# Kernel tuning notes

Measured on AMD Instinct MI355X. Metric: run time of the kernel, lower is better.

The kernel has to match this reference:

```python
import jax, jax.numpy as jnp
import numpy as np
from jax import lax

N, C, H, W = 16, 1024, 32, 32
CQK = C // 8
EPS = 1e-5


def setup_inputs() -> dict:
    key = jax.random.key(0)
    ks = jax.random.split(key, 10)
    s = lambda fan_in: 1.0 / np.sqrt(fan_in)
    return {
        "x": jax.random.normal(ks[0], (N, C, H, W), dtype=jnp.float32),
        "head_w": jax.random.uniform(ks[1], (1, C, 3, 3), jnp.float32, -s(C * 9), s(C * 9)),
        "bn_w": jnp.ones((1,), jnp.float32),
        "bn_b": jnp.zeros((1,), jnp.float32),
        "q_w": jax.random.uniform(ks[2], (CQK, C), jnp.float32, -s(C), s(C)),
        "q_b": jax.random.uniform(ks[3], (CQK,), jnp.float32, -s(C), s(C)),
        "k_w": jax.random.uniform(ks[4], (CQK, C), jnp.float32, -s(C), s(C)),
        "k_b": jax.random.uniform(ks[5], (CQK,), jnp.float32, -s(C), s(C)),
        "v_w": jax.random.uniform(ks[6], (C, C), jnp.float32, -s(C), s(C)),
        "v_b": jax.random.uniform(ks[7], (C,), jnp.float32, -s(C), s(C)),
        "gamma": jnp.ones((1,), jnp.float32),
    }


def reference(x, head_w, bn_w, bn_b, q_w, q_b, k_w, k_b, v_w, v_b, gamma):
    n, c, h, w = x.shape
    hw = h * w
    # activation head: 3x3 conv (no bias) -> BatchNorm (train mode, batch stats) -> sigmoid
    a = lax.conv_general_dilated(x, head_w, (1, 1), ((1, 1), (1, 1)),
                                 dimension_numbers=("NCHW", "OIHW", "NCHW"))  # [n,1,h,w]
    mu = jnp.mean(a, axis=(0, 2, 3), keepdims=True)
    var = jnp.mean((a - mu) ** 2, axis=(0, 2, 3), keepdims=True)
    bn = (a - mu) / jnp.sqrt(var + EPS) * bn_w.reshape(1, -1, 1, 1) + bn_b.reshape(1, -1, 1, 1)
    ccam = jax.nn.sigmoid(bn)  # [n,1,h,w]

    xf = x.reshape(n, c, hw)                 # [n,c,hw]
    cm = ccam.reshape(n, hw)                 # [n,hw]
    fg = jnp.einsum("nh,nch->nc", cm, xf) / hw
    bg = jnp.einsum("nh,nch->nc", 1.0 - cm, xf) / hw

    # self-attention with 1x1-conv projections (no 1/sqrt(d) scaling, per source)
    q = jnp.einsum("oc,nch->noh", q_w, xf) + q_b[None, :, None]  # [n,cqk,hw]
    k = jnp.einsum("oc,nch->noh", k_w, xf) + k_b[None, :, None]
    v = jnp.einsum("oc,nch->noh", v_w, xf) + v_b[None, :, None]  # [n,c,hw]
    attn = jax.nn.softmax(jnp.einsum("noi,noj->nij", q, k), axis=-1)  # [n,hw,hw]
    out = jnp.einsum("ncj,nij->nci", v, attn)                         # [n,c,hw]
    out = gamma * out + xf

    global_feats = jnp.max(out, axis=-1)  # adaptive_max_pool2d to (1,1)
    return fg, bg, ccam, global_feats
```

## Files before the change

### kernel.cpp

```cpp
#include <hip/hip_runtime.h>
#include <math.h>

typedef _Float16 f16x8 __attribute__((ext_vector_type(8)));
typedef float f32x4 __attribute__((ext_vector_type(4)));

#define NB 16
#define CC 1024
#define HW 1024
#define CQK 128
#define EPS 1e-5f

#define OFF_A     0
#define OFF_STATS 65536
#define OFF_CM    66048
#define OFF_WH    131584
#define OFF_QT    (OFF_WH + 2621440)
#define OFF_KT    (OFF_QT + 4194304)
#define OFF_V     (OFF_KT + 4194304)
#define OFF_XH    (OFF_V + 33554432)
#define OFF_ATTN  OFF_XH
#define OFF_PMAX  (OFF_ATTN + 67108864)
#define OFF_YP    OFF_V

__device__ __forceinline__ ushort f16b(float f) {
    union { _Float16 h; ushort u; } v;
    v.h = (_Float16)f;
    return v.u;
}

__device__ __forceinline__ void gl_lds16(const void* g, void* s) {
    __builtin_amdgcn_global_load_lds(
        (const __attribute__((address_space(1))) void*)g,
        (__attribute__((address_space(3))) void*)s, 16, 0, 0);
}

__global__ __launch_bounds__(256) void cvtT_x_conv(
        const float* __restrict__ x, const float* __restrict__ hwt,
        ushort* __restrict__ xh, float* __restrict__ yp) {
    int n = blockIdx.z, cb = blockIdx.y, hb = blockIdx.x;
    __shared__ float tile[32][33];
    int t = threadIdx.x;
    int r = t >> 3, c4 = (t & 7) << 2;
    const float* s = x + ((size_t)(n * CC + cb * 32 + r) << 10) + hb * 32 + c4;
    float4 v = *(const float4*)s;
    tile[r][c4] = v.x; tile[r][c4 + 1] = v.y; tile[r][c4 + 2] = v.z; tile[r][c4 + 3] = v.w;
    __syncthreads();
    int hw_l = t >> 3, cg = (t & 7) << 2;
    ushort4 h4;
    h4.x = f16b(tile[cg + 0][hw_l]); h4.y = f16b(tile[cg + 1][hw_l]);
    h4.z = f16b(tile[cg + 2][hw_l]); h4.w = f16b(tile[cg + 3][hw_l]);
    *(ushort4*)&xh[((size_t)(n * HW + hb * 32 + hw_l) << 10) + cb * 32 + cg] = h4;
    float pacc[9] = {};
    #pragma unroll
    for (int cc = 0; cc < 4; ++cc) {
        float xv = tile[cg + cc][hw_l];
        const float* w9 = hwt + (cb * 32 + cg + cc) * 9;
        #pragma unroll
        for (int tp = 0; tp < 9; ++tp) pacc[tp] += xv * w9[tp];
    }
    #pragma unroll
    for (int off = 1; off < 8; off <<= 1)
        #pragma unroll
        for (int tp = 0; tp < 9; ++tp) pacc[tp] += __shfl_xor(pacc[tp], off);
    if ((t & 7) == 0) {
        #pragma unroll
        for (int tp = 0; tp < 9; ++tp)
            yp[(((size_t)(n * 32 + cb) * 9 + tp) << 10) + hb * 32 + hw_l] = pacc[tp];
    }
}

__global__ __launch_bounds__(256) void conv_combine(
        const float* __restrict__ yp, float* __restrict__ a) {
    int idx = blockIdx.x * 256 + threadIdx.x;
    int n = idx >> 10, p = idx & 1023;
    int h = p >> 5, w = p & 31;
    float s = 0.f;
    #pragma unroll
    for (int tp = 0; tp < 9; ++tp) {
        int dy = tp / 3 - 1, dx = tp % 3 - 1;
        int hh = h + dy, ww = w + dx;
        if (hh < 0 || hh > 31 || ww < 0 || ww > 31) continue;
        int pp = (hh << 5) + ww;
        const float* b = yp + (((size_t)(n * 32) * 9) << 10) + ((size_t)tp << 10) + pp;
        #pragma unroll
        for (int cch = 0; cch < 32; ++cch) s += b[((size_t)cch * 9) << 10];
    }
    a[idx] = s;
}

__global__ void bn_stats(const float* __restrict__ a, float* __restrict__ stats) {
    int t = threadIdx.x;
    float s = 0.f, ss = 0.f;
    for (int i = t; i < NB * HW; i += 256) { float v = a[i]; s += v; ss += v * v; }
    __shared__ float rs[256], rss[256];
    rs[t] = s; rss[t] = ss;
    __syncthreads();
    for (int off = 128; off > 0; off >>= 1) {
        if (t < off) { rs[t] += rs[t + off]; rss[t] += rss[t + off]; }
        __syncthreads();
    }
    if (t == 0) {
        float mu = rs[0] / (NB * HW);
        float var = rss[0] / (NB * HW) - mu * mu;
        stats[0] = mu;
        stats[1] = rsqrtf(var + EPS);
    }
}

__global__ void ccam_kernel(const float* __restrict__ a, const float* __restrict__ stats,
                            const float* __restrict__ bn_w, const float* __restrict__ bn_b,
                            float* __restrict__ cm, float* __restrict__ out_ccam) {
    int i = blockIdx.x * 256 + threadIdx.x;
    float z = (a[i] - stats[0]) * stats[1] * bn_w[0] + bn_b[0];
    float sg = 1.f / (1.f + expf(-z));
    cm[i] = sg;
    out_ccam[i] = sg;
}

__global__ void fgbg_kernel(const float* __restrict__ x, const float* __restrict__ cm,
                            float* __restrict__ out_fg, float* __restrict__ out_bg) {
    int gid = blockIdx.x * blockDim.x + threadIdx.x;
    int wid = gid >> 6;
    int lane = threadIdx.x & 63;
    int n = wid >> 10, c = wid & 1023;
    const float* xp = x + ((size_t)(n * CC + c) << 10);
    const float* cp = cm + (n << 10);
    float sf = 0.f, sa = 0.f;
    for (int h = lane; h < HW; h += 64) { float xv = xp[h]; sf += cp[h] * xv; sa += xv; }
    for (int off = 32; off > 0; off >>= 1) { sf += __shfl_xor(sf, off); sa += __shfl_xor(sa, off); }
    if (lane == 0) {
        float fgv = sf * (1.f / HW);
        out_fg[(n << 10) + c] = fgv;
        out_bg[(n << 10) + c] = sa * (1.f / HW) - fgv;
    }
}

__global__ void cvt_w(const float* __restrict__ qw, const float* __restrict__ kw,
                      const float* __restrict__ vw, ushort* __restrict__ wh) {
    size_t e = ((size_t)blockIdx.x * 256 + threadIdx.x) * 4;
    float4 v;
    if (e < 131072)       v = *(const float4*)(qw + e);
    else if (e < 262144)  v = *(const float4*)(kw + e - 131072);
    else                  v = *(const float4*)(vw + e - 262144);
    ushort4 h4;
    h4.x = f16b(v.x); h4.y = f16b(v.y); h4.z = f16b(v.z); h4.w = f16b(v.w);
    *(ushort4*)&wh[e] = h4;
}

__device__ __forceinline__ void gemm_loop_f16(
        const ushort* __restrict__ Ag, int ap,
        const ushort* __restrict__ Bg, int bp,
        int K, ushort* lds, f32x4 acc[4][4]) {
    const int t = threadIdx.x;
    const int lane = t & 63, w = t >> 6;
    const int lr = lane & 15, kg = lane >> 4;
    const int wm = (w >> 1) << 6, wn = (w & 1) << 6;
    ushort* Ab = lds;
    ushort* Bb = lds + 8192;
    const int rowl = lane >> 3;
    const int cs = (lane & 7) ^ rowl;
    const ushort* sA = Ag + cs * 8;
    const ushort* sB = Bg + cs * 8;
    const int rb = (w << 3) + rowl;
    const int ldsb = w << 9;
    const int cA0 = kg ^ (lr & 7);
    const int cA1 = (kg | 4) ^ (lr & 7);
    for (int k0 = 0; k0 < K; k0 += 64) {
        __syncthreads();
        #pragma unroll
        for (int q = 0; q < 4; ++q) {
            int r = rb + (q << 5);
            gl_lds16(sA + (size_t)r * ap + k0, Ab + ldsb + (q << 11));
            gl_lds16(sB + (size_t)r * bp + k0, Bb + ldsb + (q << 11));
        }
        __syncthreads();
        #pragma unroll
        for (int s = 0; s < 2; ++s) {
            int ch = s ? cA1 : cA0;
            f16x8 a[4], b[4];
            #pragma unroll
            for (int i = 0; i < 4; ++i) {
                a[i] = *(const f16x8*)&Ab[((wm + i * 16 + lr) << 6) + ch * 8];
                b[i] = *(const f16x8*)&Bb[((wn + i * 16 + lr) << 6) + ch * 8];
            }
            #pragma unroll
            for (int i = 0; i < 4; ++i)
                #pragma unroll
                for (int j = 0; j < 4; ++j)
                    acc[i][j] = __builtin_amdgcn_mfma_f32_16x16x32_f16(a[i], b[j], acc[i][j], 0, 0, 0);
        }
    }
}

__global__ __launch_bounds__(256) void qkv_f16(
        const ushort* __restrict__ Wh, const ushort* __restrict__ xh,
        const float* __restrict__ qb, const float* __restrict__ kb,
        const float* __restrict__ vb,
        ushort* __restrict__ qt, ushort* __restrict__ kt, ushort* __restrict__ v) {
    __shared__ __align__(16) ushort lds[17408];
    int n = blockIdx.z, m0 = blockIdx.y << 7, j0 = blockIdx.x << 7;
    f32x4 acc[4][4];
    #pragma unroll
    for (int i = 0; i < 4; ++i)
        #pragma unroll
        for (int j = 0; j < 4; ++j) acc[i][j] = (f32x4){0.f, 0.f, 0.f, 0.f};
    gemm_loop_f16(Wh + (size_t)m0 * CC, CC,
                  xh + ((size_t)(n * HW + j0)) * CC, CC, CC, lds, acc);
    const int t = threadIdx.x, lane = t & 63, wid = t >> 6;
    const int lr = lane & 15, kg = lane >> 4;
    const int wm = (wid >> 1) << 6, wn = (wid & 1) << 6;
    if (m0 < 256) {
        ushort* dst = (m0 == 0) ? qt : kt;
        const float* bp = (m0 == 0) ? qb : kb;
        #pragma unroll
        for (int mi = 0; mi < 4; ++mi)
            #pragma unroll
            for (int nj = 0; nj < 4; ++nj) {
                int m = wm + mi * 16 + kg * 4;
                int j = j0 + wn + nj * 16 + lr;
                ushort4 pk;
                pk.x = f16b(acc[mi][nj][0] + bp[m + 0]);
                pk.y = f16b(acc[mi][nj][1] + bp[m + 1]);
                pk.z = f16b(acc[mi][nj][2] + bp[m + 2]);
                pk.w = f16b(acc[mi][nj][3] + bp[m + 3]);
                *(ushort4*)&dst[((size_t)(n * HW + j) << 7) + m] = pk;
            }
    } else {
        int mo = m0 - 256;
        __syncthreads();
        #pragma unroll
        for (int mi = 0; mi < 4; ++mi)
            #pragma unroll
            for (int nj = 0; nj < 4; ++nj) {
                int ml = wm + mi * 16 + kg * 4;
                int jl = wn + nj * 16 + lr;
                #pragma unroll
                for (int r = 0; r < 4; ++r)
                    lds[(ml + r) * 136 + jl] = f16b(acc[mi][nj][r] + vb[mo + ml + r]);
            }
        __syncthreads();
        #pragma unroll
        for (int p = 0; p < 8; ++p) {
            int row = (t >> 4) + p * 16;
            int ch = (t & 15) * 8;
            *(uint4*)&v[((size_t)(n * CC + mo + row) << 10) + j0 + ch] =
                *(const uint4*)&lds[row * 136 + ch];
        }
    }
}

__global__ __launch_bounds__(256) void score_f16(
        const ushort* __restrict__ qt, const ushort* __restrict__ kt,
        float* __restrict__ attn) {
    __shared__ __align__(16) ushort lds[16384];
    int n = blockIdx.z, i0 = blockIdx.y << 7, j0 = blockIdx.x << 7;
    f32x4 acc[4][4];
    #pragma unroll
    for (int i = 0; i < 4; ++i)
        #pragma unroll
        for (int j = 0; j < 4; ++j) acc[i][j] = (f32x4){0.f, 0.f, 0.f, 0.f};
    gemm_loop_f16(qt + ((size_t)(n * HW + i0)) * CQK, CQK,
                  kt + ((size_t)(n * HW + j0)) * CQK, CQK, CQK, lds, acc);
    const int t = threadIdx.x, lane = t & 63, wid = t >> 6;
    const int lr = lane & 15, kg = lane >> 4;
    const int wm = (wid >> 1) << 6, wn = (wid & 1) << 6;
    #pragma unroll
    for (int mi = 0; mi < 4; ++mi)
        #pragma unroll
        for (int r = 0; r < 4; ++r) {
            int irow = i0 + wm + mi * 16 + kg * 4 + r;
            #pragma unroll
            for (int nj = 0; nj < 4; ++nj) {
                int j = j0 + wn + nj * 16 + lr;
                attn[((size_t)(n * HW + irow) << 10) + j] = acc[mi][nj][r];
            }
        }
}

__global__ void softmax_f16(float* __restrict__ attn) {
    int row = blockIdx.x;
    float* p = attn + ((size_t)row << 10);
    int t = threadIdx.x;
    int wid = t >> 6, lane = t & 63;
    float vals[4];
    float m = -INFINITY;
    #pragma unroll
    for (int r = 0; r < 4; ++r) { vals[r] = p[t + (r << 8)]; m = fmaxf(m, vals[r]); }
    for (int off = 32; off > 0; off >>= 1) m = fmaxf(m, __shfl_xor(m, off));
    __shared__ float redm[4], reds[4];
    if (lane == 0) redm[wid] = m;
    __syncthreads();
    if (t == 0) {
        float mm = redm[0];
        for (int g = 1; g < 4; ++g) mm = fmaxf(mm, redm[g]);
        redm[0] = mm;
    }
    __syncthreads();
    m = redm[0];
    float s = 0.f;
    #pragma unroll
    for (int r = 0; r < 4; ++r) { vals[r] = expf(vals[r] - m); s += vals[r]; }
    for (int off = 32; off > 0; off >>= 1) s += __shfl_xor(s, off);
    if (lane == 0) reds[wid] = s;
    __syncthreads();
    if (t == 0) {
        float ss = reds[0];
        for (int g = 1; g < 4; ++g) ss += reds[g];
        reds[0] = ss;
    }
    __syncthreads();
    float inv = 1.f / reds[0];
    ushort* ph = (ushort*)p;
    #pragma unroll
    for (int r = 0; r < 4; ++r) ph[t + (r << 8)] = f16b(vals[r] * inv);
}

__global__ __launch_bounds__(256) void out_f16(
        const ushort* __restrict__ v, const ushort* __restrict__ pus,
        const float* __restrict__ x, const float* __restrict__ gamma,
        float* __restrict__ pmax) {
    __shared__ __align__(16) ushort lds[16384];
    int n = blockIdx.z, c0 = blockIdx.y << 7, i0 = blockIdx.x << 7;
    f32x4 acc[4][4];
    #pragma unroll
    for (int i = 0; i < 4; ++i)
        #pragma unroll
        for (int j = 0; j < 4; ++j) acc[i][j] = (f32x4){0.f, 0.f, 0.f, 0.f};
    gemm_loop_f16(v + ((size_t)(n * CC + c0) << 10), HW,
                  pus + ((size_t)(n * HW + i0)) * 2048, 2048, HW, lds, acc);
    const int t = threadIdx.x, lane = t & 63, wid = t >> 6;
    const int lr = lane & 15, kg = lane >> 4;
    const int wm = (wid >> 1) << 6, wn = (wid & 1) << 6;
    float g = gamma[0];
    __syncthreads();
    float (*smax)[64] = (float(*)[64])lds;
    #pragma unroll
    for (int mi = 0; mi < 4; ++mi)
        #pragma unroll
        for (int r = 0; r < 4; ++r) {
            int c = c0 + wm + mi * 16 + kg * 4 + r;
            const float* xp = x + ((size_t)(n * CC + c) << 10);
            float mx = -INFINITY;
            #pragma unroll
            for (int nj = 0; nj < 4; ++nj) {
                int i = i0 + wn + nj * 16 + lr;
                mx = fmaxf(mx, g * acc[mi][nj][r] + xp[i]);
            }
            #pragma unroll
            for (int off = 1; off < 16; off <<= 1) mx = fmaxf(mx, __shfl_xor(mx, off));
            if (lr == 0) smax[wid][mi * 16 + kg * 4 + r] = mx;
        }
    __syncthreads();
    if (t < 128) {
        int half = t >> 6, cl = t & 63;
        float m = fmaxf(smax[half * 2][cl], smax[half * 2 + 1][cl]);
        pmax[((size_t)(n * 8 + blockIdx.x) << 10) + c0 + half * 64 + cl] = m;
    }
}

__global__ void gf_reduce(const float* __restrict__ pmax, float* __restrict__ gf) {
    int idx = blockIdx.x * 256 + threadIdx.x;
    int n = idx >> 10, c = idx & 1023;
    float m = -INFINITY;
    #pragma unroll
    for (int ib = 0; ib < 8; ++ib)
        m = fmaxf(m, pmax[(((size_t)(n << 3) + ib) << 10) + c]);
    gf[idx] = m;
}

extern "C" void kernel_launch(void* const* d_in, const int* in_sizes, int n_in,
                              void* d_out, int out_size, void* d_ws, size_t ws_size,
                              hipStream_t stream) {
    const float* x      = (const float*)d_in[0];
    const float* head_w = (const float*)d_in[1];
    const float* bn_w   = (const float*)d_in[2];
    const float* bn_b   = (const float*)d_in[3];
    const float* q_w    = (const float*)d_in[4];
    const float* q_b    = (const float*)d_in[5];
    const float* k_w    = (const float*)d_in[6];
    const float* k_b    = (const float*)d_in[7];
    const float* v_w    = (const float*)d_in[8];
    const float* v_b    = (const float*)d_in[9];
    const float* gamma  = (const float*)d_in[10];

    float* out      = (float*)d_out;
    float* out_fg   = out;
    float* out_bg   = out + 16384;
    float* out_ccam = out + 32768;
    float* out_gf   = out + 49152;

    char* B = (char*)d_ws;
    float*  a     = (float*)(B + OFF_A);
    float*  stats = (float*)(B + OFF_STATS);
    float*  cm    = (float*)(B + OFF_CM);
    ushort* Wh    = (ushort*)(B + OFF_WH);
    ushort* qt    = (ushort*)(B + OFF_QT);
    ushort* kt    = (ushort*)(B + OFF_KT);
    ushort* v     = (ushort*)(B + OFF_V);
    ushort* xh    = (ushort*)(B + OFF_XH);
    float*  attn  = (float*)(B + OFF_ATTN);
    float*  pmax  = (float*)(B + OFF_PMAX);
    float*  ypart = (float*)(B + OFF_YP);

    hipLaunchKernelGGL(cvtT_x_conv, dim3(32, 32, 16), dim3(256), 0, stream, x, head_w, xh, ypart);
    hipLaunchKernelGGL(conv_combine, dim3(64), dim3(256), 0, stream, ypart, a);
    hipLaunchKernelGGL(bn_stats, dim3(1), dim3(256), 0, stream, a, stats);
    hipLaunchKernelGGL(ccam_kernel, dim3(64), dim3(256), 0, stream, a, stats, bn_w, bn_b, cm, out_ccam);
    hipLaunchKernelGGL(fgbg_kernel, dim3(4096), dim3(256), 0, stream, x, cm, out_fg, out_bg);

    hipLaunchKernelGGL(cvt_w, dim3(1280), dim3(256), 0, stream, q_w, k_w, v_w, Wh);
    hipLaunchKernelGGL(qkv_f16, dim3(8, 10, 16), dim3(256), 0, stream,
                       Wh, xh, q_b, k_b, v_b, qt, kt, v);
    hipLaunchKernelGGL(score_f16, dim3(8, 8, 16), dim3(256), 0, stream, qt, kt, attn);
    hipLaunchKernelGGL(softmax_f16, dim3(NB * HW), dim3(256), 0, stream, attn);
    hipLaunchKernelGGL(out_f16, dim3(8, 8, 16), dim3(256), 0, stream,
                       v, (const ushort*)attn, x, gamma, pmax);
    hipLaunchKernelGGL(gf_reduce, dim3(64), dim3(256), 0, stream, pmax, out_gf);
}
```

Baseline: 349.3 us.

## Double-buffer LDS tiles in the shared f16 GEMM loop and vectorize softmax/fgbg

The shared f16 MFMA GEMM loop now uses two LDS buffers. It issues the global-to-LDS loads for the next K tile before running the MFMAs on the current one, with one barrier per iteration instead of two, so memory latency can overlap with compute. The cost is that the qkv, score and out kernels each need a 64 KB LDS array, which may reduce how many blocks fit on a CU. Separately, fgbg_kernel and softmax_f16 switch to float4 loads and packed stores so each thread handles contiguous elements with wider memory transactions.

```diff
diff --git a/kernel.cpp b/kernel.cpp
--- a/kernel.cpp
+++ b/kernel.cpp
@@ -123,10 +123,16 @@
     int wid = gid >> 6;
     int lane = threadIdx.x & 63;
     int n = wid >> 10, c = wid & 1023;
-    const float* xp = x + ((size_t)(n * CC + c) << 10);
-    const float* cp = cm + (n << 10);
+    const float4* xp = (const float4*)(x + ((size_t)(n * CC + c) << 10));
+    const float4* cp = (const float4*)(cm + (n << 10));
     float sf = 0.f, sa = 0.f;
-    for (int h = lane; h < HW; h += 64) { float xv = xp[h]; sf += cp[h] * xv; sa += xv; }
+    #pragma unroll
+    for (int it = 0; it < 4; ++it) {
+        float4 xv = xp[lane + (it << 6)];
+        float4 cv = cp[lane + (it << 6)];
+        sf += xv.x * cv.x + xv.y * cv.y + xv.z * cv.z + xv.w * cv.w;
+        sa += xv.x + xv.y + xv.z + xv.w;
+    }
     for (int off = 32; off > 0; off >>= 1) { sf += __shfl_xor(sf, off); sa += __shfl_xor(sa, off); }
     if (lane == 0) {
         float fgv = sf * (1.f / HW);
@@ -155,8 +161,6 @@
     const int lane = t & 63, w = t >> 6;
     const int lr = lane & 15, kg = lane >> 4;
     const int wm = (w >> 1) << 6, wn = (w & 1) << 6;
-    ushort* Ab = lds;
-    ushort* Bb = lds + 8192;
     const int rowl = lane >> 3;
     const int cs = (lane & 7) ^ rowl;
     const ushort* sA = Ag + cs * 8;
@@ -165,15 +169,28 @@
     const int ldsb = w << 9;
     const int cA0 = kg ^ (lr & 7);
     const int cA1 = (kg | 4) ^ (lr & 7);
-    for (int k0 = 0; k0 < K; k0 += 64) {
-        __syncthreads();
-        #pragma unroll
-        for (int q = 0; q < 4; ++q) {
-            int r = rb + (q << 5);
-            gl_lds16(sA + (size_t)r * ap + k0, Ab + ldsb + (q << 11));
-            gl_lds16(sB + (size_t)r * bp + k0, Bb + ldsb + (q << 11));
+    const int nt = K >> 6;
+    #pragma unroll
+    for (int q = 0; q < 4; ++q) {
+        int r = rb + (q << 5);
+        gl_lds16(sA + (size_t)r * ap, lds + ldsb + (q << 11));
+        gl_lds16(sB + (size_t)r * bp, lds + 8192 + ldsb + (q << 11));
+    }
+    __syncthreads();
+    int buf = 0;
+    for (int tile = 0; tile < nt; ++tile) {
+        if (tile + 1 < nt) {
+            int nb = (buf ^ 1) << 14;
+            int k0 = (tile + 1) << 6;
+            #pragma unroll
+            for (int q = 0; q < 4; ++q) {
+                int r = rb + (q << 5);
+                gl_lds16(sA + (size_t)r * ap + k0, lds + nb + ldsb + (q << 11));
+                gl_lds16(sB + (size_t)r * bp + k0, lds + nb + 8192 + ldsb + (q << 11));
+            }
         }
-        __syncthreads();
+        const ushort* Ab = lds + (buf << 14);
+        const ushort* Bb = Ab + 8192;
         #pragma unroll
         for (int s = 0; s < 2; ++s) {
             int ch = s ? cA1 : cA0;
@@ -189,6 +206,8 @@
                 for (int j = 0; j < 4; ++j)
                     acc[i][j] = __builtin_amdgcn_mfma_f32_16x16x32_f16(a[i], b[j], acc[i][j], 0, 0, 0);
         }
+        __syncthreads();
+        buf ^= 1;
     }
 }
 
@@ -197,7 +216,7 @@
         const float* __restrict__ qb, const float* __restrict__ kb,
         const float* __restrict__ vb,
         ushort* __restrict__ qt, ushort* __restrict__ kt, ushort* __restrict__ v) {
-    __shared__ __align__(16) ushort lds[17408];
+    __shared__ __align__(16) ushort lds[32768];
     int n = blockIdx.z, m0 = blockIdx.y << 7, j0 = blockIdx.x << 7;
     f32x4 acc[4][4];
     #pragma unroll
@@ -252,7 +271,7 @@
 __global__ __launch_bounds__(256) void score_f16(
         const ushort* __restrict__ qt, const ushort* __restrict__ kt,
         float* __restrict__ attn) {
-    __shared__ __align__(16) ushort lds[16384];
+    __shared__ __align__(16) ushort lds[32768];
     int n = blockIdx.z, i0 = blockIdx.y << 7, j0 = blockIdx.x << 7;
     f32x4 acc[4][4];
     #pragma unroll
@@ -282,44 +301,38 @@
     float* p = attn + ((size_t)row << 10);
     int t = threadIdx.x;
     int wid = t >> 6, lane = t & 63;
-    float vals[4];
-    float m = -INFINITY;
-    #pragma unroll
-    for (int r = 0; r < 4; ++r) { vals[r] = p[t + (r << 8)]; m = fmaxf(m, vals[r]); }
+    float4 v4 = *(const float4*)&p[t << 2];
+    float m = fmaxf(fmaxf(v4.x, v4.y), fmaxf(v4.z, v4.w));
     for (int off = 32; off > 0; off >>= 1) m = fmaxf(m, __shfl_xor(m, off));
     __shared__ float redm[4], reds[4];
     if (lane == 0) redm[wid] = m;
     __syncthreads();
     if (t == 0) {
-        float mm = redm[0];
-        for (int g = 1; g < 4; ++g) mm = fmaxf(mm, redm[g]);
+        float mm = fmaxf(fmaxf(redm[0], redm[1]), fmaxf(redm[2], redm[3]));
         redm[0] = mm;
     }
     __syncthreads();
     m = redm[0];
-    float s = 0.f;
-    #pragma unroll
-    for (int r = 0; r < 4; ++r) { vals[r] = expf(vals[r] - m); s += vals[r]; }
+    v4.x = expf(v4.x - m); v4.y = expf(v4.y - m);
+    v4.z = expf(v4.z - m); v4.w = expf(v4.w - m);
+    float s = v4.x + v4.y + v4.z + v4.w;
     for (int off = 32; off > 0; off >>= 1) s += __shfl_xor(s, off);
     if (lane == 0) reds[wid] = s;
     __syncthreads();
-    if (t == 0) {
-        float ss = reds[0];
-        for (int g = 1; g < 4; ++g) ss += reds[g];
-        reds[0] = ss;
-    }
+    if (t == 0) reds[0] = reds[0] + reds[1] + reds[2] + reds[3];
     __syncthreads();
     float inv = 1.f / reds[0];
-    ushort* ph = (ushort*)p;
-    #pragma unroll
-    for (int r = 0; r < 4; ++r) ph[t + (r << 8)] = f16b(vals[r] * inv);
+    ushort4 h4;
+    h4.x = f16b(v4.x * inv); h4.y = f16b(v4.y * inv);
+    h4.z = f16b(v4.z * inv); h4.w = f16b(v4.w * inv);
+    *(ushort4*)&((ushort*)p)[t << 2] = h4;
 }
 
 __global__ __launch_bounds__(256) void out_f16(
         const ushort* __restrict__ v, const ushort* __restrict__ pus,
         const float* __restrict__ x, const float* __restrict__ gamma,
         float* __restrict__ pmax) {
-    __shared__ __align__(16) ushort lds[16384];
+    __shared__ __align__(16) ushort lds[32768];
     int n = blockIdx.z, c0 = blockIdx.y << 7, i0 = blockIdx.x << 7;
     f32x4 acc[4][4];
     #pragma unroll
```

Result: faster. 336.7 us (-3.6%).
